# Kernel optimization log

Measured on AMD Instinct MI355X. Metric: run time of the kernel, lower is better.

## Reference

```python
import jax, jax.numpy as jnp
import numpy as np

K = 16          # num_bins
BOUND = 5.0     # tail_bound
MBW = 1e-3      # min_bin_width
MBH = 1e-3      # min_bin_height
MD = 1e-3       # min_derivative


def setup_inputs() -> dict:
    key = jax.random.key(0)
    ks = jax.random.split(key, 6)
    B, N, CD, H = 4096, 1024, 64, 256
    OUT = 3 * K + 1  # 2K widths/heights + (K+1) derivatives

    def lin_w(k, fan_in, shape):
        return (jax.random.normal(k, shape, jnp.float32) / np.sqrt(fan_in)).astype(jnp.float32)

    return {
        "cond": jax.random.normal(ks[0], (B, CD), jnp.float32),
        "y": jax.random.normal(ks[1], (B, N), jnp.float32) * 2.0,
        "W1": lin_w(ks[2], CD, (CD, H)), "b1": jnp.zeros((H,), jnp.float32),
        "W2": lin_w(ks[3], H, (H, H)),   "b2": jnp.zeros((H,), jnp.float32),
        "W3": lin_w(ks[4], H, (H, OUT)), "b3": jnp.zeros((OUT,), jnp.float32),
    }


def reference(cond, y, W1, b1, W2, b2, W3, b3):
    # --- conditioner MLP (concat mode, depth=2, dropout=0 / eval) ---
    h = jax.nn.relu(cond @ W1 + b1)
    h = jax.nn.relu(h @ W2 + b2)
    p = h @ W3 + b3                      # (B, 3K+1)
    un_w, un_h, un_d = p[..., :K], p[..., K:2 * K], p[..., 2 * K:]

    left, right, bottom, top = -BOUND, BOUND, -BOUND, BOUND
    widths = MBW + (right - left - K * MBW) * jax.nn.softmax(un_w, axis=-1)    # (B, K)
    heights = MBH + (top - bottom - K * MBH) * jax.nn.softmax(un_h, axis=-1)   # (B, K)
    cumw = jnp.pad(jnp.cumsum(widths, axis=-1), ((0, 0), (1, 0))) + left       # (B, K+1)
    cumh = jnp.pad(jnp.cumsum(heights, axis=-1), ((0, 0), (1, 0))) + bottom    # (B, K+1)
    deriv = MD + jax.nn.softplus(un_d)                                         # (B, K+1)

    xc = jnp.clip(y, left, right)                                              # (B, N)
    # bin search: O(K) broadcasted compare+sum, as in the original
    bin_idx = jnp.sum(xc[..., None] >= cumw[:, None, 1:], axis=-1)             # (B, N) int
    bin_idx = jnp.clip(bin_idx, 0, K - 1)

    gat = lambda a, i: jnp.take_along_axis(a, i, axis=-1)  # (B,K')[(B,N)] -> (B,N)
    x0 = gat(cumw, bin_idx)
    w = gat(widths, bin_idx)
    y0 = gat(cumh, bin_idx)
    hh = gat(heights, bin_idx)
    d0 = gat(deriv, bin_idx)
    d1 = gat(deriv, bin_idx + 1)

    delta = hh / w
    theta = (xc - x0) / w
    omt = 1.0 - theta
    num = hh * (delta * theta * theta + d0 * theta * omt)
    den = delta + (d0 + d1 - 2.0 * delta) * theta * omt
    out = y0 + num / den

    der_num = jnp.maximum(delta * delta * (d1 * theta * theta + 2.0 * delta * theta * omt + d0 * omt * omt), 1e-12)
    der_den = jnp.maximum(den * den, 1e-12)
    logdet = jnp.log(der_num) - jnp.log(der_den)

    outside = (y < left) | (y > right)
    out = jnp.where(outside, y, out)
    logdet = jnp.where(outside, jnp.zeros_like(logdet), logdet)
    return out, logdet
```

## Files before the change

### kernel.cpp

```cpp
#include <hip/hip_runtime.h>
#include <math.h>

namespace {
constexpr int KB    = 16;
constexpr int OUTP  = 3*KB + 1;
constexpr int CDIM  = 64;
constexpr int HDIM  = 256;
constexpr int NCOL  = 1024;
constexpr int NROW  = 4096;
constexpr float BOUNDF = 5.0f;
constexpr float MBW_ = 0.001f;
constexpr float MBH_ = 0.001f;
constexpr float MD_  = 0.001f;
constexpr int PSTR  = 51;
constexpr int MROWS = 16;
constexpr int HSTR  = 260;
constexpr int N3    = 64;
constexpr int W1E = 16*2*512;
constexpr int W2E = 16*8*512;
constexpr int W3E = 4*8*512;
}

typedef __attribute__((ext_vector_type(8))) short bf16x8;
typedef __attribute__((ext_vector_type(4))) float f32x4;

__device__ __forceinline__ unsigned short f32_to_bf16_rne(float v) {
    unsigned u = __float_as_uint(v);
    return (unsigned short)((u + 0x7FFFu + ((u >> 16) & 1u)) >> 16);
}
__device__ __forceinline__ float bf16_to_f32(unsigned short h) {
    return __uint_as_float(((unsigned)h) << 16);
}
__device__ __forceinline__ void split_bf16(float v, unsigned short& hi, unsigned short& lo) {
    hi = f32_to_bf16_rne(v);
    lo = f32_to_bf16_rne(v - bf16_to_f32(hi));
}
__device__ __forceinline__ unsigned pack_split(float v) {
    unsigned short h, l; split_bf16(v, h, l);
    return (unsigned)h | ((unsigned)l << 16);
}

__global__ __launch_bounds__(256) void prep_weights(
    const float* __restrict__ W1, const float* __restrict__ W2,
    const float* __restrict__ W3,
    unsigned short* __restrict__ w1hi, unsigned short* __restrict__ w1lo,
    unsigned short* __restrict__ w2hi, unsigned short* __restrict__ w2lo,
    unsigned short* __restrict__ w3hi, unsigned short* __restrict__ w3lo)
{
    const int t = blockIdx.x * 256 + threadIdx.x;
    {
        const int j = t & 7, mrow = (t>>3)&15, kg = (t>>7)&3, c = (t>>9)&7, T = t>>12;
        const int k = c*32 + kg*8 + j, col = T*16 + mrow;
        unsigned short h, l; split_bf16(W2[(size_t)k*HDIM + col], h, l);
        w2hi[t] = h; w2lo[t] = l;
    }
    if (t < W1E) {
        const int j = t & 7, mrow = (t>>3)&15, kg = (t>>7)&3, c = (t>>9)&1, T = t>>10;
        const int k = c*32 + kg*8 + j, col = T*16 + mrow;
        unsigned short h, l; split_bf16(W1[(size_t)k*HDIM + col], h, l);
        w1hi[t] = h; w1lo[t] = l;
    }
    if (t < W3E) {
        const int j = t & 7, mrow = (t>>3)&15, kg = (t>>7)&3, c = (t>>9)&7, T = t>>12;
        const int k = c*32 + kg*8 + j, col = T*16 + mrow;
        const float v = (col < OUTP) ? W3[(size_t)k*OUTP + col] : 0.f;
        unsigned short h, l; split_bf16(v, h, l);
        w3hi[t] = h; w3lo[t] = l;
    }
}

__global__ __launch_bounds__(256) void mlp_mfma_kernel(
    const float* __restrict__ cond,
    const float* __restrict__ b1, const float* __restrict__ b2,
    const float* __restrict__ b3,
    const unsigned short* __restrict__ w1hi, const unsigned short* __restrict__ w1lo,
    const unsigned short* __restrict__ w2hi, const unsigned short* __restrict__ w2lo,
    const unsigned short* __restrict__ w3hi, const unsigned short* __restrict__ w3lo,
    float* __restrict__ params)
{
    __shared__ unsigned h1c[MROWS][HSTR];
    __shared__ unsigned h2c[MROWS][HSTR];
    __shared__ float    p_s[MROWS][OUTP];
    __shared__ float    prm_s[MROWS][PSTR];

    const int tid  = threadIdx.x;
    const int lane = tid & 63;
    const int wid  = tid >> 6;
    const int mrow = lane & 15;
    const int kg   = lane >> 4;
    const int row0 = blockIdx.x * MROWS;

    {
        f32x4 acc[4];
        #pragma unroll
        for (int t = 0; t < 4; ++t) acc[t] = (f32x4)0.f;

        #pragma unroll
        for (int c = 0; c < CDIM/32; ++c) {
            const float* ap = cond + (size_t)(row0 + mrow)*CDIM + c*32 + kg*8;
            const float4 a0 = *(const float4*)ap;
            const float4 a1 = *(const float4*)(ap + 4);
            const float av[8] = {a0.x,a0.y,a0.z,a0.w,a1.x,a1.y,a1.z,a1.w};
            bf16x8 Ahi, Alo;
            #pragma unroll
            for (int j = 0; j < 8; ++j) {
                unsigned short h, l; split_bf16(av[j], h, l);
                Ahi[j] = (short)h; Alo[j] = (short)l;
            }
            #pragma unroll
            for (int t = 0; t < 4; ++t) {
                const int T = wid*4 + t;
                const size_t off = (size_t)(T*2 + c)*512 + lane*8;
                const bf16x8 Bhi = *(const bf16x8*)(w1hi + off);
                const bf16x8 Blo = *(const bf16x8*)(w1lo + off);
                acc[t] = __builtin_amdgcn_mfma_f32_16x16x32_bf16(Alo, Bhi, acc[t], 0, 0, 0);
                acc[t] = __builtin_amdgcn_mfma_f32_16x16x32_bf16(Ahi, Blo, acc[t], 0, 0, 0);
                acc[t] = __builtin_amdgcn_mfma_f32_16x16x32_bf16(Ahi, Bhi, acc[t], 0, 0, 0);
            }
        }
        #pragma unroll
        for (int t = 0; t < 4; ++t) {
            const int col = (wid*4 + t)*16 + mrow;
            const float bb = b1[col];
            #pragma unroll
            for (int r = 0; r < 4; ++r) {
                const int row = kg*4 + r;
                const float v = fmaxf(acc[t][r] + bb, 0.f);
                h1c[row][col] = pack_split(v);
            }
        }
    }
    __syncthreads();

    {
        f32x4 acc[4];
        #pragma unroll
        for (int t = 0; t < 4; ++t) acc[t] = (f32x4)0.f;

        #pragma unroll 2
        for (int c = 0; c < HDIM/32; ++c) {
            const uint4 u0 = *(const uint4*)&h1c[mrow][c*32 + kg*8];
            const uint4 u1 = *(const uint4*)&h1c[mrow][c*32 + kg*8 + 4];
            const unsigned uu[8] = {u0.x,u0.y,u0.z,u0.w,u1.x,u1.y,u1.z,u1.w};
            bf16x8 Ahi, Alo;
            #pragma unroll
            for (int j = 0; j < 8; ++j) {
                Ahi[j] = (short)(uu[j] & 0xFFFFu);
                Alo[j] = (short)(uu[j] >> 16);
            }
            #pragma unroll
            for (int t = 0; t < 4; ++t) {
                const int T = wid*4 + t;
                const size_t off = (size_t)(T*8 + c)*512 + lane*8;
                const bf16x8 Bhi = *(const bf16x8*)(w2hi + off);
                const bf16x8 Blo = *(const bf16x8*)(w2lo + off);
                acc[t] = __builtin_amdgcn_mfma_f32_16x16x32_bf16(Alo, Bhi, acc[t], 0, 0, 0);
                acc[t] = __builtin_amdgcn_mfma_f32_16x16x32_bf16(Ahi, Blo, acc[t], 0, 0, 0);
                acc[t] = __builtin_amdgcn_mfma_f32_16x16x32_bf16(Ahi, Bhi, acc[t], 0, 0, 0);
            }
        }
        #pragma unroll
        for (int t = 0; t < 4; ++t) {
            const int col = (wid*4 + t)*16 + mrow;
            const float bb = b2[col];
            #pragma unroll
            for (int r = 0; r < 4; ++r) {
                const int row = kg*4 + r;
                const float v = fmaxf(acc[t][r] + bb, 0.f);
                h2c[row][col] = pack_split(v);
            }
        }
    }
    __syncthreads();

    {
        f32x4 acc = (f32x4)0.f;
        #pragma unroll 2
        for (int c = 0; c < HDIM/32; ++c) {
            const uint4 u0 = *(const uint4*)&h2c[mrow][c*32 + kg*8];
            const uint4 u1 = *(const uint4*)&h2c[mrow][c*32 + kg*8 + 4];
            const unsigned uu[8] = {u0.x,u0.y,u0.z,u0.w,u1.x,u1.y,u1.z,u1.w};
            bf16x8 Ahi, Alo;
            #pragma unroll
            for (int j = 0; j < 8; ++j) {
                Ahi[j] = (short)(uu[j] & 0xFFFFu);
                Alo[j] = (short)(uu[j] >> 16);
            }
            const size_t off = (size_t)(wid*8 + c)*512 + lane*8;
            const bf16x8 Bhi = *(const bf16x8*)(w3hi + off);
            const bf16x8 Blo = *(const bf16x8*)(w3lo + off);
            acc = __builtin_amdgcn_mfma_f32_16x16x32_bf16(Alo, Bhi, acc, 0, 0, 0);
            acc = __builtin_amdgcn_mfma_f32_16x16x32_bf16(Ahi, Blo, acc, 0, 0, 0);
            acc = __builtin_amdgcn_mfma_f32_16x16x32_bf16(Ahi, Bhi, acc, 0, 0, 0);
        }
        const int col = wid*16 + mrow;
        if (col < OUTP) {
            const float bb = b3[col];
            #pragma unroll
            for (int r = 0; r < 4; ++r)
                p_s[kg*4 + r][col] = acc[r] + bb;
        }
    }
    __syncthreads();

    if (tid < MROWS*3) {
        const int r   = tid / 3;
        const int seg = tid - 3*r;
        if (seg < 2) {
            const int   off   = (seg == 0) ? 0 : KB;
            const int   cbase = (seg == 0) ? 0 : 17;
            const float mb    = (seg == 0) ? MBW_ : MBH_;
            float m = -1e30f;
            #pragma unroll
            for (int i = 0; i < KB; ++i) m = fmaxf(m, p_s[r][off+i]);
            float e[KB];
            float s = 0.f;
            #pragma unroll
            for (int i = 0; i < KB; ++i) { e[i] = __expf(p_s[r][off+i] - m); s += e[i]; }
            const float span = (2.f*BOUNDF - (float)KB*mb) / s;
            float c = -BOUNDF;
            prm_s[r][cbase] = c;
            #pragma unroll
            for (int i = 0; i < KB; ++i) {
                c += mb + span*e[i];
                prm_s[r][cbase + 1 + i] = c;
            }
        } else {
            #pragma unroll
            for (int i = 0; i < KB+1; ++i) {
                const float x  = p_s[r][2*KB + i];
                const float sp = (x > 20.f) ? x : __logf(1.f + __expf(x));
                prm_s[r][34 + i] = MD_ + sp;
            }
        }
    }
    __syncthreads();

    for (int i = tid; i < MROWS*PSTR; i += 256)
        params[(size_t)row0*PSTR + i] = (&prm_s[0][0])[i];
}

__global__ __launch_bounds__(256) void spline_kernel(
    const float* __restrict__ y,
    const float* __restrict__ params,
    float* __restrict__ out,
    float* __restrict__ logdet)
{
    __shared__ float prm[PSTR];
    __shared__ float rec[KB][8];
    __shared__ float scan_s[KB];

    const int b   = blockIdx.x;
    const int tid = threadIdx.x;
    if (tid < PSTR) prm[tid] = params[(size_t)b*PSTR + tid];
    __syncthreads();
    if (tid < KB) {
        const int k = tid;
        rec[k][0] = prm[k];        rec[k][1] = prm[k+1];
        rec[k][2] = prm[17+k];     rec[k][3] = prm[17+k+1];
        rec[k][4] = prm[34+k];     rec[k][5] = prm[34+k+1];
        rec[k][6] = 0.f;           rec[k][7] = 0.f;
        scan_s[k] = prm[k+1];
    }
    __syncthreads();

    float cw[KB];
    #pragma unroll
    for (int q = 0; q < 4; ++q) {
        const float4 t4 = *(const float4*)&scan_s[4*q];
        cw[4*q+0] = t4.x; cw[4*q+1] = t4.y; cw[4*q+2] = t4.z; cw[4*q+3] = t4.w;
    }

    const size_t base = (size_t)b * NCOL + 4*tid;
    const float4 yv   = *(const float4*)(y + base);
    const float  yy[4] = {yv.x, yv.y, yv.z, yv.w};
    float ov[4], lv[4];

    #pragma unroll
    for (int i = 0; i < 4; ++i) {
        const float yi = yy[i];
        const bool outside = (yi < -BOUNDF) || (yi > BOUNDF);
        const float xc = fminf(fmaxf(yi, -BOUNDF), BOUNDF);
        int bin = 0;
        #pragma unroll
        for (int k = 0; k < KB; ++k) bin += (xc >= cw[k]) ? 1 : 0;
        bin = min(bin, KB-1);

        const float4 lo = *(const float4*)&rec[bin][0];
        const float2 hi = *(const float2*)&rec[bin][4];
        const float w  = lo.y - lo.x;
        const float hh = lo.w - lo.z;
        const float d0 = hi.x, d1 = hi.y;

        const float inv_w = __fdividef(1.f, w);
        const float delta = hh * inv_w;
        const float theta = (xc - lo.x) * inv_w;
        const float omt   = 1.f - theta;
        const float tt    = theta * theta;
        const float tomt  = theta * omt;
        const float num   = hh * (delta*tt + d0*tomt);
        const float den   = delta + (d0 + d1 - 2.f*delta)*tomt;
        const float o     = lo.z + __fdividef(num, den);
        const float der_num = fmaxf(delta*delta*(d1*tt + 2.f*delta*tomt + d0*omt*omt), 1e-12f);
        const float der_den = fmaxf(den*den, 1e-12f);
        const float ld      = __logf(__fdividef(der_num, der_den));

        ov[i] = outside ? yi : o;
        lv[i] = outside ? 0.f : ld;
    }

    *(float4*)(out + base)    = make_float4(ov[0], ov[1], ov[2], ov[3]);
    *(float4*)(logdet + base) = make_float4(lv[0], lv[1], lv[2], lv[3]);
}

extern "C" void kernel_launch(void* const* d_in, const int* in_sizes, int n_in,
                              void* d_out, int out_size, void* d_ws, size_t ws_size,
                              hipStream_t stream) {
    const float* cond = (const float*)d_in[0];
    const float* y    = (const float*)d_in[1];
    const float* W1   = (const float*)d_in[2];
    const float* b1   = (const float*)d_in[3];
    const float* W2   = (const float*)d_in[4];
    const float* b2   = (const float*)d_in[5];
    const float* W3   = (const float*)d_in[6];
    const float* b3   = (const float*)d_in[7];

    float* out    = (float*)d_out;
    float* logdet = out + (size_t)NROW * NCOL;

    float* params = (float*)d_ws;
    unsigned short* w1hi = (unsigned short*)((char*)d_ws + (1 << 20));
    unsigned short* w1lo = w1hi + W1E;
    unsigned short* w2hi = w1lo + W1E;
    unsigned short* w2lo = w2hi + W2E;
    unsigned short* w3hi = w2lo + W2E;
    unsigned short* w3lo = w3hi + W3E;

    prep_weights<<<256, 256, 0, stream>>>(W1, W2, W3, w1hi, w1lo, w2hi, w2lo, w3hi, w3lo);
    mlp_mfma_kernel<<<NROW/MROWS, 256, 0, stream>>>(cond, b1, b2, b3,
                                                    w1hi, w1lo, w2hi, w2lo, w3hi, w3lo,
                                                    params);
    spline_kernel<<<NROW, 256, 0, stream>>>(y, params, out, logdet);
}
```

Measured before the change: 41.38 us.

## Fuse conditioner MLP and spline evaluation into one 512-thread kernel

Merges the MLP kernel and the per-row spline kernel into one kernel, so spline parameters stay in shared memory instead of round-tripping through a global workspace and a third launch is avoided. Block size doubles to 512 threads: layers 1-2 split column tiles across 8 waves, layer 3 uses only 4 waves, and each thread then evaluates 8 rows of the 16-row tile. The cost is only 256 blocks for the elementwise spline phase, with y loads no longer overlapped across many small blocks, plus higher register and LDS pressure per block.

```diff
diff --git a/kernel.cpp b/kernel.cpp
--- a/kernel.cpp
+++ b/kernel.cpp
@@ -15,7 +15,6 @@
 constexpr int PSTR  = 51;
 constexpr int MROWS = 16;
 constexpr int HSTR  = 260;
-constexpr int N3    = 64;
 constexpr int W1E = 16*2*512;
 constexpr int W2E = 16*8*512;
 constexpr int W3E = 4*8*512;
@@ -69,19 +68,21 @@
     }
 }
 
-__global__ __launch_bounds__(256) void mlp_mfma_kernel(
-    const float* __restrict__ cond,
+__global__ __launch_bounds__(512) void fused_mfma_spline(
+    const float* __restrict__ cond, const float* __restrict__ y,
     const float* __restrict__ b1, const float* __restrict__ b2,
     const float* __restrict__ b3,
     const unsigned short* __restrict__ w1hi, const unsigned short* __restrict__ w1lo,
     const unsigned short* __restrict__ w2hi, const unsigned short* __restrict__ w2lo,
     const unsigned short* __restrict__ w3hi, const unsigned short* __restrict__ w3lo,
-    float* __restrict__ params)
+    float* __restrict__ out, float* __restrict__ logdet)
 {
     __shared__ unsigned h1c[MROWS][HSTR];
     __shared__ unsigned h2c[MROWS][HSTR];
     __shared__ float    p_s[MROWS][OUTP];
     __shared__ float    prm_s[MROWS][PSTR];
+    __shared__ float    rec[MROWS][KB][8];
+    __shared__ float    scan_s[MROWS][16];
 
     const int tid  = threadIdx.x;
     const int lane = tid & 63;
@@ -91,10 +92,8 @@
     const int row0 = blockIdx.x * MROWS;
 
     {
-        f32x4 acc[4];
-        #pragma unroll
-        for (int t = 0; t < 4; ++t) acc[t] = (f32x4)0.f;
-
+        f32x4 acc[2];
+        acc[0] = (f32x4)0.f; acc[1] = (f32x4)0.f;
         #pragma unroll
         for (int c = 0; c < CDIM/32; ++c) {
             const float* ap = cond + (size_t)(row0 + mrow)*CDIM + c*32 + kg*8;
@@ -108,8 +107,8 @@
                 Ahi[j] = (short)h; Alo[j] = (short)l;
             }
             #pragma unroll
-            for (int t = 0; t < 4; ++t) {
-                const int T = wid*4 + t;
+            for (int t = 0; t < 2; ++t) {
+                const int T = 2*wid + t;
                 const size_t off = (size_t)(T*2 + c)*512 + lane*8;
                 const bf16x8 Bhi = *(const bf16x8*)(w1hi + off);
                 const bf16x8 Blo = *(const bf16x8*)(w1lo + off);
@@ -119,24 +118,19 @@
             }
         }
         #pragma unroll
-        for (int t = 0; t < 4; ++t) {
-            const int col = (wid*4 + t)*16 + mrow;
+        for (int t = 0; t < 2; ++t) {
+            const int col = (2*wid + t)*16 + mrow;
             const float bb = b1[col];
             #pragma unroll
-            for (int r = 0; r < 4; ++r) {
-                const int row = kg*4 + r;
-                const float v = fmaxf(acc[t][r] + bb, 0.f);
-                h1c[row][col] = pack_split(v);
-            }
+            for (int r = 0; r < 4; ++r)
+                h1c[kg*4 + r][col] = pack_split(fmaxf(acc[t][r] + bb, 0.f));
         }
     }
     __syncthreads();
 
     {
-        f32x4 acc[4];
-        #pragma unroll
-        for (int t = 0; t < 4; ++t) acc[t] = (f32x4)0.f;
-
+        f32x4 acc[2];
+        acc[0] = (f32x4)0.f; acc[1] = (f32x4)0.f;
         #pragma unroll 2
         for (int c = 0; c < HDIM/32; ++c) {
             const uint4 u0 = *(const uint4*)&h1c[mrow][c*32 + kg*8];
@@ -149,8 +143,8 @@
                 Alo[j] = (short)(uu[j] >> 16);
             }
             #pragma unroll
-            for (int t = 0; t < 4; ++t) {
-                const int T = wid*4 + t;
+            for (int t = 0; t < 2; ++t) {
+                const int T = 2*wid + t;
                 const size_t off = (size_t)(T*8 + c)*512 + lane*8;
                 const bf16x8 Bhi = *(const bf16x8*)(w2hi + off);
                 const bf16x8 Blo = *(const bf16x8*)(w2lo + off);
@@ -160,20 +154,17 @@
             }
         }
         #pragma unroll
-        for (int t = 0; t < 4; ++t) {
-            const int col = (wid*4 + t)*16 + mrow;
+        for (int t = 0; t < 2; ++t) {
+            const int col = (2*wid + t)*16 + mrow;
             const float bb = b2[col];
             #pragma unroll
-            for (int r = 0; r < 4; ++r) {
-                const int row = kg*4 + r;
-                const float v = fmaxf(acc[t][r] + bb, 0.f);
-                h2c[row][col] = pack_split(v);
-            }
-        }
-    }
-    __syncthreads();
-
-    {
+            for (int r = 0; r < 4; ++r)
+                h2c[kg*4 + r][col] = pack_split(fmaxf(acc[t][r] + bb, 0.f));
+        }
+    }
+    __syncthreads();
+
+    if (wid < 4) {
         f32x4 acc = (f32x4)0.f;
         #pragma unroll 2
         for (int c = 0; c < HDIM/32; ++c) {
@@ -236,81 +227,72 @@
     }
     __syncthreads();
 
-    for (int i = tid; i < MROWS*PSTR; i += 256)
-        params[(size_t)row0*PSTR + i] = (&prm_s[0][0])[i];
-}
-
-__global__ __launch_bounds__(256) void spline_kernel(
-    const float* __restrict__ y,
-    const float* __restrict__ params,
-    float* __restrict__ out,
-    float* __restrict__ logdet)
-{
-    __shared__ float prm[PSTR];
-    __shared__ float rec[KB][8];
-    __shared__ float scan_s[KB];
-
-    const int b   = blockIdx.x;
-    const int tid = threadIdx.x;
-    if (tid < PSTR) prm[tid] = params[(size_t)b*PSTR + tid];
-    __syncthreads();
-    if (tid < KB) {
-        const int k = tid;
-        rec[k][0] = prm[k];        rec[k][1] = prm[k+1];
-        rec[k][2] = prm[17+k];     rec[k][3] = prm[17+k+1];
-        rec[k][4] = prm[34+k];     rec[k][5] = prm[34+k+1];
-        rec[k][6] = 0.f;           rec[k][7] = 0.f;
-        scan_s[k] = prm[k+1];
-    }
-    __syncthreads();
-
-    float cw[KB];
+    if (tid < MROWS*KB) {
+        const int r = tid >> 4;
+        const int k = tid & 15;
+        rec[r][k][0] = prm_s[r][k];        rec[r][k][1] = prm_s[r][k+1];
+        rec[r][k][2] = prm_s[r][17+k];     rec[r][k][3] = prm_s[r][17+k+1];
+        rec[r][k][4] = prm_s[r][34+k];     rec[r][k][5] = prm_s[r][34+k+1];
+        rec[r][k][6] = 0.f;                rec[r][k][7] = 0.f;
+        scan_s[r][k] = prm_s[r][k+1];
+    }
+    __syncthreads();
+
+    const int rowp = tid >> 8;
+    const int col0 = (tid & 255) * 4;
+
+    float4 yv[8];
     #pragma unroll
-    for (int q = 0; q < 4; ++q) {
-        const float4 t4 = *(const float4*)&scan_s[4*q];
-        cw[4*q+0] = t4.x; cw[4*q+1] = t4.y; cw[4*q+2] = t4.z; cw[4*q+3] = t4.w;
-    }
-
-    const size_t base = (size_t)b * NCOL + 4*tid;
-    const float4 yv   = *(const float4*)(y + base);
-    const float  yy[4] = {yv.x, yv.y, yv.z, yv.w};
-    float ov[4], lv[4];
+    for (int p = 0; p < 8; ++p)
+        yv[p] = *(const float4*)(y + (size_t)(row0 + 2*p + rowp)*NCOL + col0);
 
     #pragma unroll
-    for (int i = 0; i < 4; ++i) {
-        const float yi = yy[i];
-        const bool outside = (yi < -BOUNDF) || (yi > BOUNDF);
-        const float xc = fminf(fmaxf(yi, -BOUNDF), BOUNDF);
-        int bin = 0;
-        #pragma unroll
-        for (int k = 0; k < KB; ++k) bin += (xc >= cw[k]) ? 1 : 0;
-        bin = min(bin, KB-1);
-
-        const float4 lo = *(const float4*)&rec[bin][0];
-        const float2 hi = *(const float2*)&rec[bin][4];
-        const float w  = lo.y - lo.x;
-        const float hh = lo.w - lo.z;
-        const float d0 = hi.x, d1 = hi.y;
-
-        const float inv_w = __fdividef(1.f, w);
-        const float delta = hh * inv_w;
-        const float theta = (xc - lo.x) * inv_w;
-        const float omt   = 1.f - theta;
-        const float tt    = theta * theta;
-        const float tomt  = theta * omt;
-        const float num   = hh * (delta*tt + d0*tomt);
-        const float den   = delta + (d0 + d1 - 2.f*delta)*tomt;
-        const float o     = lo.z + __fdividef(num, den);
-        const float der_num = fmaxf(delta*delta*(d1*tt + 2.f*delta*tomt + d0*omt*omt), 1e-12f);
-        const float der_den = fmaxf(den*den, 1e-12f);
-        const float ld      = __logf(__fdividef(der_num, der_den));
-
-        ov[i] = outside ? yi : o;
-        lv[i] = outside ? 0.f : ld;
-    }
-
-    *(float4*)(out + base)    = make_float4(ov[0], ov[1], ov[2], ov[3]);
-    *(float4*)(logdet + base) = make_float4(lv[0], lv[1], lv[2], lv[3]);
+    for (int p = 0; p < 8; ++p) {
+        const int r = 2*p + rowp;
+        float cw[KB];
+        #pragma unroll
+        for (int q = 0; q < 4; ++q) {
+            const float4 t4 = *(const float4*)&scan_s[r][4*q];
+            cw[4*q+0] = t4.x; cw[4*q+1] = t4.y; cw[4*q+2] = t4.z; cw[4*q+3] = t4.w;
+        }
+        const float yy[4] = {yv[p].x, yv[p].y, yv[p].z, yv[p].w};
+        float ov[4], lv[4];
+        #pragma unroll
+        for (int i = 0; i < 4; ++i) {
+            const float yi = yy[i];
+            const bool outside = (yi < -BOUNDF) || (yi > BOUNDF);
+            const float xc = fminf(fmaxf(yi, -BOUNDF), BOUNDF);
+            int bin = 0;
+            #pragma unroll
+            for (int k = 0; k < KB; ++k) bin += (xc >= cw[k]) ? 1 : 0;
+            bin = min(bin, KB-1);
+
+            const float4 lo = *(const float4*)&rec[r][bin][0];
+            const float2 hi = *(const float2*)&rec[r][bin][4];
+            const float w  = lo.y - lo.x;
+            const float hh = lo.w - lo.z;
+            const float d0 = hi.x, d1 = hi.y;
+
+            const float inv_w = __fdividef(1.f, w);
+            const float delta = hh * inv_w;
+            const float theta = (xc - lo.x) * inv_w;
+            const float omt   = 1.f - theta;
+            const float tt    = theta * theta;
+            const float tomt  = theta * omt;
+            const float num   = hh * (delta*tt + d0*tomt);
+            const float den   = delta + (d0 + d1 - 2.f*delta)*tomt;
+            const float o     = lo.z + __fdividef(num, den);
+            const float der_num = fmaxf(delta*delta*(d1*tt + 2.f*delta*tomt + d0*omt*omt), 1e-12f);
+            const float der_den = fmaxf(den*den, 1e-12f);
+            const float ld      = __logf(__fdividef(der_num, der_den));
+
+            ov[i] = outside ? yi : o;
+            lv[i] = outside ? 0.f : ld;
+        }
+        const size_t base = (size_t)(row0 + r)*NCOL + col0;
+        *(float4*)(out + base)    = make_float4(ov[0], ov[1], ov[2], ov[3]);
+        *(float4*)(logdet + base) = make_float4(lv[0], lv[1], lv[2], lv[3]);
+    }
 }
 
 extern "C" void kernel_launch(void* const* d_in, const int* in_sizes, int n_in,
@@ -328,8 +310,7 @@
     float* out    = (float*)d_out;
     float* logdet = out + (size_t)NROW * NCOL;
 
-    float* params = (float*)d_ws;
-    unsigned short* w1hi = (unsigned short*)((char*)d_ws + (1 << 20));
+    unsigned short* w1hi = (unsigned short*)d_ws;
     unsigned short* w1lo = w1hi + W1E;
     unsigned short* w2hi = w1lo + W1E;
     unsigned short* w2lo = w2hi + W2E;
@@ -337,8 +318,7 @@
     unsigned short* w3lo = w3hi + W3E;
 
     prep_weights<<<256, 256, 0, stream>>>(W1, W2, W3, w1hi, w1lo, w2hi, w2lo, w3hi, w3lo);
-    mlp_mfma_kernel<<<NROW/MROWS, 256, 0, stream>>>(cond, b1, b2, b3,
-                                                    w1hi, w1lo, w2hi, w2lo, w3hi, w3lo,
-                                                    params);
-    spline_kernel<<<NROW, 256, 0, stream>>>(y, params, out, logdet);
-}
+    fused_mfma_spline<<<NROW/MROWS, 512, 0, stream>>>(cond, y, b1, b2, b3,
+                                                      w1hi, w1lo, w2hi, w2lo, w3hi, w3lo,
+                                                      out, logdet);
+}
```

Measured after the change: 38.51 us. 1.07x faster.
